# Kernel tuning notes

Hardware: AMD Instinct MI355X
Metric: run time of the kernel (lower is better)

## Reference

```python
import jax, jax.numpy as jnp
import numpy as np

IN_SIZE = 1024
OUT_SIZE = 4096
RANK = 4
NSTACK = (OUT_SIZE + IN_SIZE - 1) // IN_SIZE  # 4


def setup_inputs() -> dict:
    key = jax.random.key(0)
    k1, k2, k3, k4 = jax.random.split(key, 4)
    init_std = float(np.sqrt(1.0 / (RANK * IN_SIZE)))
    x = jax.random.normal(k1, (2, 2048, IN_SIZE), dtype=jnp.float32)
    G = jax.random.normal(k2, (NSTACK, RANK, IN_SIZE), dtype=jnp.float32) * init_std
    H = jax.random.normal(k3, (NSTACK, RANK, IN_SIZE), dtype=jnp.float32) * init_std
    bound = 1.0 / float(np.sqrt(IN_SIZE))
    bias = jax.random.uniform(k4, (OUT_SIZE,), dtype=jnp.float32, minval=-bound, maxval=bound)
    return {"x": x, "G": G, "H": H, "bias": bias}


def reference(x, G, H, bias):
    n = x.shape[-1]
    nstack, rank, _ = G.shape
    out_size = bias.shape[0]
    u = x.reshape(-1, n)                     # (B, n) flattened tokens
    # Stage 1: circular conv of reversed input with H filters (zero-padded to 2n)
    u_f = jnp.fft.rfft(u[:, ::-1], n=2 * n, axis=-1)        # (B, n+1) complex
    H_f = jnp.fft.rfft(H, n=2 * n, axis=-1)                 # (nstack, rank, n+1)
    uv_f = u_f[:, None, None, :] * H_f                       # (B, nstack, rank, n+1)
    # irfft(..., 2n)[..., reverse_idx] == first n samples reversed
    tr = jnp.fft.irfft(uv_f, n=2 * n, axis=-1)[..., :n][..., ::-1]  # (B, nstack, rank, n)
    # Stage 2: conv with G filters, summed over rank
    w_f = jnp.fft.rfft(tr, n=2 * n, axis=-1)                # (B, nstack, rank, n+1)
    G_f = jnp.fft.rfft(G, n=2 * n, axis=-1)                 # (nstack, rank, n+1)
    wv_sum_f = jnp.einsum('bsrf,srf->bsf', w_f, G_f)        # sum over rank
    out = jnp.fft.irfft(wv_sum_f, n=2 * n, axis=-1)[..., :n]  # (B, nstack, n)
    out = out.reshape(u.shape[0], nstack * n)[:, :out_size] + bias
    return out.reshape(x.shape[:-1] + (out_size,))
```

## Files before the change

kernel.cpp:

```cpp
#include <hip/hip_runtime.h>
#include <hip/hip_bf16.h>

#define NSTACK 4
#define RANK 4
#define NIN 1024
#define NOUT 4096
#define NTOK 4096

typedef __bf16 bf16x8 __attribute__((ext_vector_type(8)));
typedef float f32x4 __attribute__((ext_vector_type(4)));

__global__ __launch_bounds__(256) void cast_x_kernel(const float* __restrict__ x,
                                                     __bf16* __restrict__ y) {
  int i = (blockIdx.x * 256 + threadIdx.x) * 8;
  float4 a = *reinterpret_cast<const float4*>(x + i);
  float4 b = *reinterpret_cast<const float4*>(x + i + 4);
  bf16x8 o;
  o[0] = (__bf16)a.x; o[1] = (__bf16)a.y; o[2] = (__bf16)a.z; o[3] = (__bf16)a.w;
  o[4] = (__bf16)b.x; o[5] = (__bf16)b.y; o[6] = (__bf16)b.z; o[7] = (__bf16)b.w;
  *reinterpret_cast<bf16x8*>(y + i) = o;
}

__global__ __launch_bounds__(256) void build_m_kernel(const float* __restrict__ G,
                                                      const float* __restrict__ H,
                                                      __bf16* __restrict__ M) {
  const int ndiag = 2 * NIN - 1;
  int wid = blockIdx.x * 4 + (threadIdx.x >> 6);
  if (wid >= NSTACK * ndiag) return;
  int lane = threadIdx.x & 63;
  int s = wid / ndiag;
  int dd = wid % ndiag;
  int d = dd - (NIN - 1);
  int ad = d < 0 ? -d : d;
  int L = NIN - ad;
  int gofs = d < 0 ? -d : 0;
  int hofs = d > 0 ? d : 0;
  const float* Gs = G + s * (RANK * NIN);
  const float* Hs = H + s * (RANK * NIN);
  __bf16* Ms = M + (size_t)s * NIN * NIN;

  float carry = 0.f;
  for (int r0 = 0; r0 < L; r0 += 64) {
    int k = r0 + lane;
    float e = 0.f;
    if (k < L) {
      int gi = k + gofs, hi = k + hofs;
      e = Gs[gi] * Hs[hi]
        + Gs[NIN + gi] * Hs[NIN + hi]
        + Gs[2 * NIN + gi] * Hs[2 * NIN + hi]
        + Gs[3 * NIN + gi] * Hs[3 * NIN + hi];
    }
    float v = e;
    #pragma unroll
    for (int off = 1; off < 64; off <<= 1) {
      float o = __shfl_up(v, off, 64);
      if (lane >= off) v += o;
    }
    if (k < L) {
      int t = k + gofs;
      int c = k + hofs;
      Ms[(size_t)t * NIN + c] = (__bf16)(carry + v);
    }
    carry += __shfl(v, 63, 64);
  }
}

__device__ __forceinline__ void gload16(const void* gsrc, void* lds) {
  __builtin_amdgcn_global_load_lds(
      (const __attribute__((address_space(1))) unsigned int*)gsrc,
      (__attribute__((address_space(3))) unsigned int*)lds, 16, 0, 0);
}

__global__ __launch_bounds__(256, 2) void gemm_bt_kernel(
    const __bf16* __restrict__ A,
    const __bf16* __restrict__ B,
    const float* __restrict__ bias,
    float* __restrict__ C) {
  __shared__ __align__(16) char smem[16384];

  const int tid = threadIdx.x;
  const int lane = tid & 63;
  const int wid = tid >> 6;
  const int wr = wid >> 1, wc = wid & 1;
  const int bn = blockIdx.x, bm = blockIdx.y;
  const int brow = bm * 128, bcol = bn * 128;

  const int b1 = tid * 16;
  const int b2 = b1 + 4096;
  const char* Ag1 = (const char*)A + (size_t)(brow + (b1 >> 6)) * (NIN * 2) + (b1 & 63);
  const char* Ag2 = (const char*)A + (size_t)(brow + (b2 >> 6)) * (NIN * 2) + (b2 & 63);
  const char* Bg1 = (const char*)B + (size_t)(bcol + (b1 >> 6)) * (NIN * 2) + (b1 & 63);
  const char* Bg2 = (const char*)B + (size_t)(bcol + (b2 >> 6)) * (NIN * 2) + (b2 & 63);
  char* lA1 = smem + b1;
  char* lA2 = smem + b2;
  char* lB1 = smem + 8192 + b1;
  char* lB2 = smem + 8192 + b2;

  const int koff = (lane >> 4) * 16;
  int aoff[4], boff[4];
  #pragma unroll
  for (int mi = 0; mi < 4; ++mi)
    aoff[mi] = (wr * 64 + mi * 16 + (lane & 15)) * 64 + koff;
  #pragma unroll
  for (int ni = 0; ni < 4; ++ni)
    boff[ni] = 8192 + (wc * 64 + ni * 16 + (lane & 15)) * 64 + koff;

  f32x4 acc[4][4];
  #pragma unroll
  for (int i = 0; i < 4; ++i)
    #pragma unroll
    for (int j = 0; j < 4; ++j)
      acc[i][j] = (f32x4){0.f, 0.f, 0.f, 0.f};

  #pragma unroll 1
  for (int kt = 0; kt < NIN / 32; ++kt) {
    const int kb = kt * 64;
    gload16(Ag1 + kb, lA1);
    gload16(Ag2 + kb, lA2);
    gload16(Bg1 + kb, lB1);
    gload16(Bg2 + kb, lB2);
    __syncthreads();

    bf16x8 af[4], bf[4];
    #pragma unroll
    for (int mi = 0; mi < 4; ++mi)
      af[mi] = *reinterpret_cast<const bf16x8*>(smem + aoff[mi]);
    #pragma unroll
    for (int ni = 0; ni < 4; ++ni)
      bf[ni] = *reinterpret_cast<const bf16x8*>(smem + boff[ni]);

    #pragma unroll
    for (int mi = 0; mi < 4; ++mi)
      #pragma unroll
      for (int ni = 0; ni < 4; ++ni)
        acc[mi][ni] = __builtin_amdgcn_mfma_f32_16x16x32_bf16(af[mi], bf[ni], acc[mi][ni], 0, 0, 0);

    __syncthreads();
  }

  #pragma unroll
  for (int ni = 0; ni < 4; ++ni) {
    const int col = bcol + wc * 64 + ni * 16 + (lane & 15);
    const float bv = bias[col];
    #pragma unroll
    for (int mi = 0; mi < 4; ++mi) {
      const int row0 = brow + wr * 64 + mi * 16 + ((lane >> 4) << 2);
      float* Cp = C + (size_t)row0 * NOUT + col;
      Cp[0 * (size_t)NOUT] = acc[mi][ni][0] + bv;
      Cp[1 * (size_t)NOUT] = acc[mi][ni][1] + bv;
      Cp[2 * (size_t)NOUT] = acc[mi][ni][2] + bv;
      Cp[3 * (size_t)NOUT] = acc[mi][ni][3] + bv;
    }
  }
}

extern "C" void kernel_launch(void* const* d_in, const int* in_sizes, int n_in,
                              void* d_out, int out_size, void* d_ws, size_t ws_size,
                              hipStream_t stream) {
  const float* x = (const float*)d_in[0];
  const float* G = (const float*)d_in[1];
  const float* H = (const float*)d_in[2];
  const float* bias = (const float*)d_in[3];
  float* out = (float*)d_out;

  __bf16* xb = (__bf16*)d_ws;
  __bf16* Mb = (__bf16*)((char*)d_ws + (size_t)NTOK * NIN * 2);

  cast_x_kernel<<<(NTOK * NIN) / (256 * 8), 256, 0, stream>>>(x, xb);
  build_m_kernel<<<(NSTACK * (2 * NIN - 1) + 3) / 4, 256, 0, stream>>>(G, H, Mb);
  gemm_bt_kernel<<<dim3(NOUT / 128, NTOK / 128), 256, 0, stream>>>(xb, Mb, bias, out);
}
```

Baseline: 149.1 us.

## Merge prep kernels and rewrite GEMM with 256x256 tiles and triple-buffered LDS

Merges the x cast and the M-matrix construction into one launch, removing a kernel launch. Rewrites the GEMM to use 256x256 block tiles with 512 threads and three LDS buffers fed by direct global-to-LDS loads issued two k-steps ahead. It also XOR-swizzles the LDS layout to avoid bank conflicts, remaps block IDs for L2 locality, and raises wave priority around the MFMA bursts. Larger tiles give more reuse per load, but the 96KB of LDS per block limits occupancy, and the hand-placed waitcnt and barrier ordering is fragile.

Measured after the change: 145.8 us. -2.2%, faster.

```diff
diff --git a/kernel.cpp b/kernel.cpp
--- a/kernel.cpp
+++ b/kernel.cpp
@@ -1,31 +1,34 @@
 #include <hip/hip_runtime.h>
 #include <hip/hip_bf16.h>
 
-#define NSTACK 4
-#define RANK 4
 #define NIN 1024
 #define NOUT 4096
 #define NTOK 4096
+#define NSTACK 4
+#define RANK 4
 
 typedef __bf16 bf16x8 __attribute__((ext_vector_type(8)));
 typedef float f32x4 __attribute__((ext_vector_type(4)));
 
-__global__ __launch_bounds__(256) void cast_x_kernel(const float* __restrict__ x,
-                                                     __bf16* __restrict__ y) {
-  int i = (blockIdx.x * 256 + threadIdx.x) * 8;
-  float4 a = *reinterpret_cast<const float4*>(x + i);
-  float4 b = *reinterpret_cast<const float4*>(x + i + 4);
-  bf16x8 o;
-  o[0] = (__bf16)a.x; o[1] = (__bf16)a.y; o[2] = (__bf16)a.z; o[3] = (__bf16)a.w;
-  o[4] = (__bf16)b.x; o[5] = (__bf16)b.y; o[6] = (__bf16)b.z; o[7] = (__bf16)b.w;
-  *reinterpret_cast<bf16x8*>(y + i) = o;
-}
-
-__global__ __launch_bounds__(256) void build_m_kernel(const float* __restrict__ G,
-                                                      const float* __restrict__ H,
-                                                      __bf16* __restrict__ M) {
+__global__ __launch_bounds__(256) void prep_kernel(const float* __restrict__ x,
+                                                   const float* __restrict__ G,
+                                                   const float* __restrict__ H,
+                                                   __bf16* __restrict__ xb,
+                                                   __bf16* __restrict__ M) {
+  int bid = blockIdx.x;
+  if (bid < 2048) {
+    int i = (bid * 256 + threadIdx.x) * 8;
+    float4 a = *reinterpret_cast<const float4*>(x + i);
+    float4 b = *reinterpret_cast<const float4*>(x + i + 4);
+    bf16x8 o;
+    o[0] = (__bf16)a.x; o[1] = (__bf16)a.y; o[2] = (__bf16)a.z; o[3] = (__bf16)a.w;
+    o[4] = (__bf16)b.x; o[5] = (__bf16)b.y; o[6] = (__bf16)b.z; o[7] = (__bf16)b.w;
+    *reinterpret_cast<bf16x8*>(xb + i) = o;
+    return;
+  }
+  bid -= 2048;
   const int ndiag = 2 * NIN - 1;
-  int wid = blockIdx.x * 4 + (threadIdx.x >> 6);
+  int wid = bid * 4 + (threadIdx.x >> 6);
   if (wid >= NSTACK * ndiag) return;
   int lane = threadIdx.x & 63;
   int s = wid / ndiag;
@@ -44,11 +47,11 @@
     int k = r0 + lane;
     float e = 0.f;
     if (k < L) {
-      int gi = k + gofs, hi = k + hofs;
-      e = Gs[gi] * Hs[hi]
-        + Gs[NIN + gi] * Hs[NIN + hi]
-        + Gs[2 * NIN + gi] * Hs[2 * NIN + hi]
-        + Gs[3 * NIN + gi] * Hs[3 * NIN + hi];
+      int gi = k + gofs, hi2 = k + hofs;
+      e = Gs[gi] * Hs[hi2]
+        + Gs[NIN + gi] * Hs[NIN + hi2]
+        + Gs[2 * NIN + gi] * Hs[2 * NIN + hi2]
+        + Gs[3 * NIN + gi] * Hs[3 * NIN + hi2];
     }
     float v = e;
     #pragma unroll
@@ -56,100 +59,153 @@
       float o = __shfl_up(v, off, 64);
       if (lane >= off) v += o;
     }
-    if (k < L) {
-      int t = k + gofs;
-      int c = k + hofs;
-      Ms[(size_t)t * NIN + c] = (__bf16)(carry + v);
-    }
+    if (k < L) Ms[(size_t)(k + gofs) * NIN + (k + hofs)] = (__bf16)(carry + v);
     carry += __shfl(v, 63, 64);
   }
 }
 
-__device__ __forceinline__ void gload16(const void* gsrc, void* lds) {
+#define BM 256
+#define BN 256
+#define BK 32
+#define ABY (BM * BK * 2)
+#define BUFBY (2 * ABY)
+#define KT (NIN / BK)
+
+__device__ __forceinline__ void gload16(const char* gsrc, char* lds) {
   __builtin_amdgcn_global_load_lds(
       (const __attribute__((address_space(1))) unsigned int*)gsrc,
       (__attribute__((address_space(3))) unsigned int*)lds, 16, 0, 0);
 }
 
-__global__ __launch_bounds__(256, 2) void gemm_bt_kernel(
+#define MEMF asm volatile("" ::: "memory")
+__device__ __forceinline__ void wgbar() {
+  MEMF; __builtin_amdgcn_s_barrier(); MEMF;
+}
+
+__global__ __launch_bounds__(512, 2) void gemm_kernel(
     const __bf16* __restrict__ A,
     const __bf16* __restrict__ B,
     const float* __restrict__ bias,
     float* __restrict__ C) {
-  __shared__ __align__(16) char smem[16384];
+  __shared__ __align__(16) char smem[3 * BUFBY];
 
   const int tid = threadIdx.x;
   const int lane = tid & 63;
+  const int lo = lane & 15;
+  const int hi = lane >> 4;
   const int wid = tid >> 6;
-  const int wr = wid >> 1, wc = wid & 1;
-  const int bn = blockIdx.x, bm = blockIdx.y;
-  const int brow = bm * 128, bcol = bn * 128;
-
-  const int b1 = tid * 16;
-  const int b2 = b1 + 4096;
-  const char* Ag1 = (const char*)A + (size_t)(brow + (b1 >> 6)) * (NIN * 2) + (b1 & 63);
-  const char* Ag2 = (const char*)A + (size_t)(brow + (b2 >> 6)) * (NIN * 2) + (b2 & 63);
-  const char* Bg1 = (const char*)B + (size_t)(bcol + (b1 >> 6)) * (NIN * 2) + (b1 & 63);
-  const char* Bg2 = (const char*)B + (size_t)(bcol + (b2 >> 6)) * (NIN * 2) + (b2 & 63);
-  char* lA1 = smem + b1;
-  char* lA2 = smem + b2;
-  char* lB1 = smem + 8192 + b1;
-  char* lB2 = smem + 8192 + b2;
-
-  const int koff = (lane >> 4) * 16;
-  int aoff[4], boff[4];
-  #pragma unroll
-  for (int mi = 0; mi < 4; ++mi)
-    aoff[mi] = (wr * 64 + mi * 16 + (lane & 15)) * 64 + koff;
-  #pragma unroll
-  for (int ni = 0; ni < 4; ++ni)
-    boff[ni] = 8192 + (wc * 64 + ni * 16 + (lane & 15)) * 64 + koff;
-
-  f32x4 acc[4][4];
-  #pragma unroll
-  for (int i = 0; i < 4; ++i)
+  const int wr = wid >> 2;
+  const int wc = wid & 3;
+
+  const int orig = blockIdx.x;
+  const int wg = (orig & 7) * 32 + (orig >> 3);
+  const int bx = wg & 15;
+  const int by = wg >> 4;
+  const int brow = by * BM;
+  const int bcol = bx * BN;
+
+  const char* Ab = (const char*)(A + (size_t)brow * NIN);
+  const char* Bb = (const char*)(B + (size_t)bcol * NIN);
+  size_t ag[2], bg[2];
+  int al[2], bl[2];
+  #pragma unroll
+  for (int l = 0; l < 2; ++l) {
+    int P = (l * 512 + tid) * 16;
+    int row = P >> 6;
+    int inner = (P & 63) ^ (((row >> 1) & 3) << 4);
+    al[l] = P;
+    ag[l] = (size_t)row * (NIN * 2) + inner;
+    bl[l] = P;
+    bg[l] = (size_t)row * (NIN * 2) + inner;
+  }
+
+  const int kso = ((hi ^ ((lo >> 1) & 3)) << 4);
+  const int abase = (wr * 128 + lo) * 64 + kso;
+  const int bbase = ABY + (wc * 64 + lo) * 64 + kso;
+
+  f32x4 acc[8][4];
+  #pragma unroll
+  for (int i = 0; i < 8; ++i)
     #pragma unroll
     for (int j = 0; j < 4; ++j)
       acc[i][j] = (f32x4){0.f, 0.f, 0.f, 0.f};
 
+  #pragma unroll
+  for (int l = 0; l < 2; ++l) gload16(Ab + ag[l], smem + al[l]);
+  #pragma unroll
+  for (int l = 0; l < 2; ++l) gload16(Bb + bg[l], smem + ABY + bl[l]);
+  #pragma unroll
+  for (int l = 0; l < 2; ++l) gload16(Ab + 64 + ag[l], smem + BUFBY + al[l]);
+  #pragma unroll
+  for (int l = 0; l < 2; ++l) gload16(Bb + 64 + bg[l], smem + BUFBY + ABY + bl[l]);
+  asm volatile("s_waitcnt vmcnt(4)" ::: "memory");
+  wgbar();
+
+  int cb = 0;
+  int sb = 2 * BUFBY;
   #pragma unroll 1
-  for (int kt = 0; kt < NIN / 32; ++kt) {
-    const int kb = kt * 64;
-    gload16(Ag1 + kb, lA1);
-    gload16(Ag2 + kb, lA2);
-    gload16(Bg1 + kb, lB1);
-    gload16(Bg2 + kb, lB2);
-    __syncthreads();
-
-    bf16x8 af[4], bf[4];
-    #pragma unroll
-    for (int mi = 0; mi < 4; ++mi)
-      af[mi] = *reinterpret_cast<const bf16x8*>(smem + aoff[mi]);
+  for (int kt = 0; kt < KT; ++kt) {
+    const char* buf = smem + cb;
+    const int kg = (kt + 2) * 64;
+    const bool dost = (kt + 2) < KT;
+
+    bf16x8 af[4], bfr[4];
+    #pragma unroll
+    for (int mi = 0; mi < 4; ++mi)
+      af[mi] = *(const bf16x8*)(buf + abase + mi * 1024);
     #pragma unroll
     for (int ni = 0; ni < 4; ++ni)
-      bf[ni] = *reinterpret_cast<const bf16x8*>(smem + boff[ni]);
-
+      bfr[ni] = *(const bf16x8*)(buf + bbase + ni * 1024);
+    if (dost) {
+      gload16(Ab + kg + ag[0], smem + sb + al[0]);
+      gload16(Ab + kg + ag[1], smem + sb + al[1]);
+    }
+    wgbar();
+    __builtin_amdgcn_s_setprio(1);
     #pragma unroll
     for (int mi = 0; mi < 4; ++mi)
       #pragma unroll
       for (int ni = 0; ni < 4; ++ni)
-        acc[mi][ni] = __builtin_amdgcn_mfma_f32_16x16x32_bf16(af[mi], bf[ni], acc[mi][ni], 0, 0, 0);
-
-    __syncthreads();
+        acc[mi][ni] = __builtin_amdgcn_mfma_f32_16x16x32_bf16(af[mi], bfr[ni], acc[mi][ni], 0, 0, 0);
+    __builtin_amdgcn_s_setprio(0);
+    wgbar();
+
+    bf16x8 af2[4];
+    #pragma unroll
+    for (int mi = 0; mi < 4; ++mi)
+      af2[mi] = *(const bf16x8*)(buf + abase + (mi + 4) * 1024);
+    if (dost) {
+      gload16(Bb + kg + bg[0], smem + sb + ABY + bl[0]);
+      gload16(Bb + kg + bg[1], smem + sb + ABY + bl[1]);
+    }
+    if (kt < KT - 2) asm volatile("s_waitcnt vmcnt(4)" ::: "memory");
+    else             asm volatile("s_waitcnt vmcnt(0)" ::: "memory");
+    wgbar();
+    __builtin_amdgcn_s_setprio(1);
+    #pragma unroll
+    for (int mi = 0; mi < 4; ++mi)
+      #pragma unroll
+      for (int ni = 0; ni < 4; ++ni)
+        acc[mi + 4][ni] = __builtin_amdgcn_mfma_f32_16x16x32_bf16(af2[mi], bfr[ni], acc[mi + 4][ni], 0, 0, 0);
+    __builtin_amdgcn_s_setprio(0);
+    wgbar();
+
+    cb += BUFBY; if (cb == 3 * BUFBY) cb = 0;
+    sb += BUFBY; if (sb == 3 * BUFBY) sb = 0;
   }
 
   #pragma unroll
   for (int ni = 0; ni < 4; ++ni) {
-    const int col = bcol + wc * 64 + ni * 16 + (lane & 15);
+    const int col = bcol + wc * 64 + ni * 16 + lo;
     const float bv = bias[col];
     #pragma unroll
-    for (int mi = 0; mi < 4; ++mi) {
-      const int row0 = brow + wr * 64 + mi * 16 + ((lane >> 4) << 2);
+    for (int mi = 0; mi < 8; ++mi) {
+      const int row0 = brow + wr * 128 + mi * 16 + hi * 4;
       float* Cp = C + (size_t)row0 * NOUT + col;
-      Cp[0 * (size_t)NOUT] = acc[mi][ni][0] + bv;
-      Cp[1 * (size_t)NOUT] = acc[mi][ni][1] + bv;
-      Cp[2 * (size_t)NOUT] = acc[mi][ni][2] + bv;
-      Cp[3 * (size_t)NOUT] = acc[mi][ni][3] + bv;
+      Cp[0]                  = acc[mi][ni][0] + bv;
+      Cp[(size_t)NOUT]       = acc[mi][ni][1] + bv;
+      Cp[2 * (size_t)NOUT]   = acc[mi][ni][2] + bv;
+      Cp[3 * (size_t)NOUT]   = acc[mi][ni][3] + bv;
     }
   }
 }
@@ -166,7 +222,6 @@
   __bf16* xb = (__bf16*)d_ws;
   __bf16* Mb = (__bf16*)((char*)d_ws + (size_t)NTOK * NIN * 2);
 
-  cast_x_kernel<<<(NTOK * NIN) / (256 * 8), 256, 0, stream>>>(x, xb);
-  build_m_kernel<<<(NSTACK * (2 * NIN - 1) + 3) / 4, 256, 0, stream>>>(G, H, Mb);
-  gemm_bt_kernel<<<dim3(NOUT / 128, NTOK / 128), 256, 0, stream>>>(xb, Mb, bias, out);
-}
+  prep_kernel<<<2048 + 2047, 256, 0, stream>>>(x, G, H, xb, Mb);
+  gemm_kernel<<<256, 512, 0, stream>>>(xb, Mb, bias, out);
+}
```
